# Optimization experiments

Measured on AMD Instinct MI355X. Metric: run time of the kernel, lower is better.

The kernel has to match this reference:

```python
import jax, jax.numpy as jnp
import numpy as np

B, T, D, H, N = 16, 512, 256, 4, 10
DK = D // H
EPS = 1e-12  # espnet LayerNorm eps


def _pe(t, d):
    # espnet PositionalEncoding table
    pos = np.arange(t, dtype=np.float32)[:, None]
    div = np.exp(np.arange(0, d, 2, dtype=np.float32) * (-np.log(10000.0) / d))
    pe = np.zeros((t, d), dtype=np.float32)
    pe[:, 0::2] = np.sin(pos * div)
    pe[:, 1::2] = np.cos(pos * div)
    return jnp.asarray(pe)


def _ln(x, g, b):
    m = jnp.mean(x, -1, keepdims=True)
    v = jnp.var(x, -1, keepdims=True)
    return (x - m) * jax.lax.rsqrt(v + EPS) * g + b


def _forward(x, x_lengths, lids, Wq, bq, Wk, bk, Wv, bv, Wo, bo, W1, b1, W2, b2, g1, be1, g2, be2, gf, bef):
    b, t, d = x.shape
    pe = _pe(t, d)
    pad = jnp.arange(t)[None, :] < x_lengths[:, None]          # [b,t] non-pad mask
    amask = pad[:, None, None, :]                               # [b,1,1,t] key mask
    onehot = (lids[:, None] == jnp.arange(N)[None, :]).astype(x.dtype)  # [b,N]
    h0 = x * np.float32(np.sqrt(d)) + pe[None]                  # scaled input + pos-enc (shared across experts)
    neg = jnp.finfo(x.dtype).min
    out = jnp.zeros_like(x)
    for z in range(N):  # fixed small set of structurally-distinct experts
        # pre-norm self-attention block
        hn = _ln(h0, g1[z], be1[z])
        q = (hn @ Wq[z] + bq[z]).reshape(b, t, H, DK).transpose(0, 2, 1, 3)
        k_ = (hn @ Wk[z] + bk[z]).reshape(b, t, H, DK).transpose(0, 2, 1, 3)
        v_ = (hn @ Wv[z] + bv[z]).reshape(b, t, H, DK).transpose(0, 2, 1, 3)
        scores = jnp.einsum('bhqd,bhkd->bhqk', q, k_) / np.float32(np.sqrt(DK))
        attn = jax.nn.softmax(jnp.where(amask, scores, neg), axis=-1)
        attn = jnp.where(amask, attn, jnp.zeros((), x.dtype))
        ctx = jnp.einsum('bhqk,bhkd->bhqd', attn, v_).transpose(0, 2, 1, 3).reshape(b, t, d)
        h = h0 + ctx @ Wo[z] + bo[z]
        # pre-norm feed-forward block
        hn2 = _ln(h, g2[z], be2[z])
        h = h + jax.nn.relu(hn2 @ W1[z] + b1[z]) @ W2[z] + b2[z]
        # final after_norm, then one-hot masked combine (== emb_lang sum)
        out = out + onehot[:, z, None, None] * _ln(h, gf[z], bef[z])
    return out


def setup_inputs() -> dict:
    key = jax.random.key(0)
    ks = jax.random.split(key, 12)
    s = np.float32(0.02)
    FF = 4 * D
    return {
        'x': jax.random.normal(ks[0], (B, T, D), jnp.float32),
        'x_lengths': jax.random.randint(ks[1], (B,), T // 2, T + 1),
        'lids': jax.random.randint(ks[2], (B,), 0, N),
        'Wq': jax.random.normal(ks[3], (N, D, D), jnp.float32) * s,
        'bq': jnp.zeros((N, D), jnp.float32),
        'Wk': jax.random.normal(ks[4], (N, D, D), jnp.float32) * s,
        'bk': jnp.zeros((N, D), jnp.float32),
        'Wv': jax.random.normal(ks[5], (N, D, D), jnp.float32) * s,
        'bv': jnp.zeros((N, D), jnp.float32),
        'Wo': jax.random.normal(ks[6], (N, D, D), jnp.float32) * s,
        'bo': jnp.zeros((N, D), jnp.float32),
        'W1': jax.random.normal(ks[7], (N, D, FF), jnp.float32) * s,
        'b1': jnp.zeros((N, FF), jnp.float32),
        'W2': jax.random.normal(ks[8], (N, FF, D), jnp.float32) * s,
        'b2': jnp.zeros((N, D), jnp.float32),
        'g1': jnp.ones((N, D), jnp.float32),
        'be1': jnp.zeros((N, D), jnp.float32),
        'g2': jnp.ones((N, D), jnp.float32),
        'be2': jnp.zeros((N, D), jnp.float32),
        'gf': jnp.ones((N, D), jnp.float32),
        'bef': jnp.zeros((N, D), jnp.float32),
    }


def reference(x, x_lengths, lids, Wq, bq, Wk, bk, Wv, bv, Wo, bo, W1, b1, W2, b2, g1, be1, g2, be2, gf, bef):
    return _forward(x, x_lengths, lids, Wq, bq, Wk, bk, Wv, bv, Wo, bo, W1, b1, W2, b2, g1, be1, g2, be2, gf, bef)
```

## Files before the change

kernel.cpp:

```cpp
#include <hip/hip_runtime.h>

typedef unsigned short u16;
typedef __bf16 bf16x8 __attribute__((ext_vector_type(8)));
typedef float  f32x4  __attribute__((ext_vector_type(4)));
typedef unsigned int   u32x4 __attribute__((ext_vector_type(4)));
typedef unsigned short u16x4 __attribute__((ext_vector_type(4)));

#define DEV __device__ __forceinline__

#define NB   16
#define TT   512
#define DD   256
#define HH   4
#define DKH  64
#define NLANG 10
#define FFD  1024

DEV u16 f2bf(float f) {
  unsigned int u = __builtin_bit_cast(unsigned int, f);
  return (u16)((u + 0x7fffu + ((u >> 16) & 1u)) >> 16);
}

DEV f32x4 zero4() { f32x4 z; z[0]=0.f; z[1]=0.f; z[2]=0.f; z[3]=0.f; return z; }

typedef __attribute__((address_space(1))) const unsigned int g_as1;
typedef __attribute__((address_space(3))) unsigned int l_as3;
DEV void load_lds16(const void* g, void* l) {
  __builtin_amdgcn_global_load_lds((g_as1*)g, (l_as3*)l, 16, 0, 0);
}

__global__ __launch_bounds__(256) void pre_kernel(
    const float* __restrict__ Wq, const float* __restrict__ Wk,
    const float* __restrict__ Wv, const float* __restrict__ Wo,
    const float* __restrict__ W1, const float* __restrict__ W2,
    u16* __restrict__ wtq, u16* __restrict__ wtk, u16* __restrict__ wtv,
    u16* __restrict__ wto, u16* __restrict__ wt1, u16* __restrict__ wt2,
    const float* __restrict__ x, float* __restrict__ h0, u16* __restrict__ hn,
    const float* __restrict__ g, const float* __restrict__ be,
    const int* __restrict__ lids) {
  __shared__ u16 tile[32][33];
  const int bx = blockIdx.x;
  if (bx < 7680) {
    const float* src; u16* dst; int R, C, z, r0, c0;
    if (bx < 2560) {
      const int w = bx / 640, rem = bx % 640;
      src = (w == 0) ? Wq : (w == 1) ? Wk : (w == 2) ? Wv : Wo;
      dst = (w == 0) ? wtq : (w == 1) ? wtk : (w == 2) ? wtv : wto;
      R = 256; C = 256; z = rem >> 6;
      const int rc = rem & 63; r0 = (rc >> 3) * 32; c0 = (rc & 7) * 32;
    } else if (bx < 5120) {
      const int rem = bx - 2560; src = W1; dst = wt1; R = 256; C = 1024;
      z = rem >> 8; const int rc = rem & 255; r0 = (rc >> 5) * 32; c0 = (rc & 31) * 32;
    } else {
      const int rem = bx - 5120; src = W2; dst = wt2; R = 1024; C = 256;
      z = rem >> 8; const int rc = rem & 255; r0 = (rc >> 3) * 32; c0 = (rc & 7) * 32;
    }
    const float* s = src + (size_t)z * R * C;
    u16* d = dst + (size_t)z * R * C;
    const int tx = threadIdx.x & 31, ty = threadIdx.x >> 5;
#pragma unroll
    for (int rr = 0; rr < 4; ++rr) {
      const int r = ty + rr * 8;
      tile[r][tx] = f2bf(s[(size_t)(r0 + r) * C + c0 + tx]);
    }
    __syncthreads();
#pragma unroll
    for (int rr = 0; rr < 4; ++rr) {
      const int cc = ty + rr * 8;
      d[(size_t)(c0 + cc) * R + r0 + tx] = tile[tx][cc];
    }
  } else {
    const int wave = threadIdx.x >> 6, lane = threadIdx.x & 63;
    const int row = (bx - 7680) * 4 + wave;
    const int b = row >> 9, t = row & 511;
    const int z = lids[b];
    const int c0 = lane * 4;
    const float4 xv = *(const float4*)(x + (size_t)row * DD + c0);
    const float kPE = -9.21034037197618f / 256.0f;
    float div0 = __expf(kPE * (float)c0);
    float div1 = __expf(kPE * (float)(c0 + 2));
    float a0 = div0 * (float)t, a1 = div1 * (float)t;
    float h[4];
    h[0] = xv.x * 16.0f + sinf(a0);
    h[1] = xv.y * 16.0f + cosf(a0);
    h[2] = xv.z * 16.0f + sinf(a1);
    h[3] = xv.w * 16.0f + cosf(a1);
    float s = h[0] + h[1] + h[2] + h[3];
    float ss = h[0]*h[0] + h[1]*h[1] + h[2]*h[2] + h[3]*h[3];
#pragma unroll
    for (int d = 1; d < 64; d <<= 1) { s += __shfl_xor(s, d); ss += __shfl_xor(ss, d); }
    float mean = s * (1.0f / 256.0f);
    float var  = ss * (1.0f / 256.0f) - mean * mean;
    float rstd = rsqrtf(var + 1e-12f);
    *(float4*)(h0 + (size_t)row * DD + c0) = make_float4(h[0], h[1], h[2], h[3]);
    u16x4 o;
#pragma unroll
    for (int j = 0; j < 4; ++j)
      o[j] = f2bf((h[j] - mean) * rstd * g[z * DD + c0 + j] + be[z * DD + c0 + j]);
    *(u16x4*)(hn + (size_t)row * DD + c0) = o;
  }
}

template<int OUTF32>
__global__ __launch_bounds__(256) void ln_kernel(const float* __restrict__ in,
                                                 void* __restrict__ outp,
                                                 const float* __restrict__ g,
                                                 const float* __restrict__ be,
                                                 const int* __restrict__ lids) {
  const int wave = threadIdx.x >> 6, lane = threadIdx.x & 63;
  const int row = blockIdx.x * 4 + wave;
  const int b = row >> 9;
  const int z = lids[b];
  const int c0 = lane * 4;
  const float4 v = *(const float4*)(in + (size_t)row * DD + c0);
  float h[4] = {v.x, v.y, v.z, v.w};
  float s = h[0] + h[1] + h[2] + h[3];
  float ss = h[0]*h[0] + h[1]*h[1] + h[2]*h[2] + h[3]*h[3];
#pragma unroll
  for (int d = 1; d < 64; d <<= 1) { s += __shfl_xor(s, d); ss += __shfl_xor(ss, d); }
  float mean = s * (1.0f / 256.0f);
  float var  = ss * (1.0f / 256.0f) - mean * mean;
  float rstd = rsqrtf(var + 1e-12f);
  if (OUTF32) {
    float4 o;
    o.x = (h[0] - mean) * rstd * g[z * DD + c0 + 0] + be[z * DD + c0 + 0];
    o.y = (h[1] - mean) * rstd * g[z * DD + c0 + 1] + be[z * DD + c0 + 1];
    o.z = (h[2] - mean) * rstd * g[z * DD + c0 + 2] + be[z * DD + c0 + 2];
    o.w = (h[3] - mean) * rstd * g[z * DD + c0 + 3] + be[z * DD + c0 + 3];
    *(float4*)((float*)outp + (size_t)row * DD + c0) = o;
  } else {
    u16x4 o;
#pragma unroll
    for (int j = 0; j < 4; ++j)
      o[j] = f2bf((h[j] - mean) * rstd * g[z * DD + c0 + j] + be[z * DD + c0 + j]);
    *(u16x4*)((u16*)outp + (size_t)row * DD + c0) = o;
  }
}

DEV void gemm_tile(const u16* __restrict__ A, const u16* __restrict__ W, int K,
                   int m0, int n0, u16* Alds, u16* Blds, f32x4 acc[4][4]) {
  const int tid = threadIdx.x;
  const int lane = tid & 63;
  const int wave = tid >> 6;
  const int wm = wave >> 1, wn = wave & 1;
  const int l15 = lane & 15, lhi = lane >> 4;
  const int srow = tid >> 3;
  const int sc8 = (tid & 7) << 3;
  for (int k0 = 0; k0 < K; k0 += 64) {
#pragma unroll
    for (int it = 0; it < 4; ++it) {
      int r = srow + it * 32;
      *(u32x4*)(Alds + r * 72 + sc8) = *(const u32x4*)(A + (size_t)(m0 + r) * K + k0 + sc8);
      *(u32x4*)(Blds + r * 72 + sc8) = *(const u32x4*)(W + (size_t)(n0 + r) * K + k0 + sc8);
    }
    __syncthreads();
#pragma unroll
    for (int ks = 0; ks < 2; ++ks) {
      const int kk = ks * 32 + lhi * 8;
      bf16x8 af[4], bfr[4];
#pragma unroll
      for (int m = 0; m < 4; ++m)
        af[m] = *(const bf16x8*)(Alds + (wm * 64 + m * 16 + l15) * 72 + kk);
#pragma unroll
      for (int n = 0; n < 4; ++n)
        bfr[n] = *(const bf16x8*)(Blds + (wn * 64 + n * 16 + l15) * 72 + kk);
#pragma unroll
      for (int m = 0; m < 4; ++m)
#pragma unroll
        for (int n = 0; n < 4; ++n)
          acc[m][n] = __builtin_amdgcn_mfma_f32_16x16x32_bf16(af[m], bfr[n], acc[m][n], 0, 0, 0);
    }
    __syncthreads();
  }
}

template<int EPI>
__global__ __launch_bounds__(256) void gemm_kernel(const u16* __restrict__ A,
                                                   const u16* __restrict__ Wt,
                                                   const float* __restrict__ bias,
                                                   const float* __restrict__ res,
                                                   void* __restrict__ outp,
                                                   const int* __restrict__ lids,
                                                   int N, int K) {
  __shared__ u16 Alds[128 * 72];
  __shared__ u16 Blds[128 * 72];
  const int b = blockIdx.z;
  const int z = lids[b];
  const int m0 = blockIdx.y * 128, n0 = blockIdx.x * 128;
  f32x4 acc[4][4];
#pragma unroll
  for (int i = 0; i < 4; ++i)
#pragma unroll
    for (int j = 0; j < 4; ++j) acc[i][j] = zero4();
  gemm_tile(A + (size_t)b * TT * K, Wt + (size_t)z * N * K, K, m0, n0, Alds, Blds, acc);
  const int lane = threadIdx.x & 63, wave = threadIdx.x >> 6;
  const int wm = wave >> 1, wn = wave & 1;
  const int l15 = lane & 15, lhi = lane >> 4;
  float bvv[4];
#pragma unroll
  for (int n = 0; n < 4; ++n) bvv[n] = bias[(size_t)z * N + n0 + wn * 64 + n * 16 + l15];
#pragma unroll
  for (int m = 0; m < 4; ++m) {
    const int grow = m0 + wm * 64 + m * 16 + lhi * 4;
#pragma unroll
    for (int n = 0; n < 4; ++n) {
      const int gcol = n0 + wn * 64 + n * 16 + l15;
#pragma unroll
      for (int r = 0; r < 4; ++r) {
        float v = acc[m][n][r] + bvv[n];
        size_t idx = (size_t)b * TT * N + (size_t)(grow + r) * N + gcol;
        if (EPI == 1) ((u16*)outp)[idx] = f2bf(v > 0.f ? v : 0.f);
        else ((u16*)outp)[idx] = f2bf(v);
      }
    }
  }
}

__global__ __launch_bounds__(256) void gemm64_kernel(const u16* __restrict__ A,
                                                     const u16* __restrict__ Wt,
                                                     const float* __restrict__ bias,
                                                     const float* __restrict__ res,
                                                     float* __restrict__ outp,
                                                     const int* __restrict__ lids,
                                                     int N, int K) {
  __shared__ u16 Alds[128 * 72];
  __shared__ u16 Blds[64 * 72];
  const int b = blockIdx.z;
  const int z = lids[b];
  const int m0 = blockIdx.y * 128, n0 = blockIdx.x * 64;
  const int tid = threadIdx.x, lane = tid & 63, wave = tid >> 6;
  const int l15 = lane & 15, lhi = lane >> 4;
  const int srow = tid >> 3, sc8 = (tid & 7) << 3;
  const u16* Ab = A + (size_t)b * TT * K;
  const u16* Wb = Wt + (size_t)z * N * K;
  f32x4 acc[2][4];
#pragma unroll
  for (int i = 0; i < 2; ++i)
#pragma unroll
    for (int j = 0; j < 4; ++j) acc[i][j] = zero4();
  for (int k0 = 0; k0 < K; k0 += 64) {
#pragma unroll
    for (int it = 0; it < 4; ++it) {
      int r = srow + it * 32;
      *(u32x4*)(Alds + r * 72 + sc8) = *(const u32x4*)(Ab + (size_t)(m0 + r) * K + k0 + sc8);
    }
#pragma unroll
    for (int it = 0; it < 2; ++it) {
      int r = srow + it * 32;
      *(u32x4*)(Blds + r * 72 + sc8) = *(const u32x4*)(Wb + (size_t)(n0 + r) * K + k0 + sc8);
    }
    __syncthreads();
#pragma unroll
    for (int ks = 0; ks < 2; ++ks) {
      const int kk = ks * 32 + lhi * 8;
      bf16x8 af[2], bfr[4];
#pragma unroll
      for (int m = 0; m < 2; ++m)
        af[m] = *(const bf16x8*)(Alds + (wave * 32 + m * 16 + l15) * 72 + kk);
#pragma unroll
      for (int n = 0; n < 4; ++n)
        bfr[n] = *(const bf16x8*)(Blds + (n * 16 + l15) * 72 + kk);
#pragma unroll
      for (int m = 0; m < 2; ++m)
#pragma unroll
        for (int n = 0; n < 4; ++n)
          acc[m][n] = __builtin_amdgcn_mfma_f32_16x16x32_bf16(af[m], bfr[n], acc[m][n], 0, 0, 0);
    }
    __syncthreads();
  }
  float bvv[4];
#pragma unroll
  for (int n = 0; n < 4; ++n) bvv[n] = bias[(size_t)z * N + n0 + n * 16 + l15];
#pragma unroll
  for (int m = 0; m < 2; ++m) {
    const int grow = m0 + wave * 32 + m * 16 + lhi * 4;
#pragma unroll
    for (int n = 0; n < 4; ++n) {
      const int gcol = n0 + n * 16 + l15;
#pragma unroll
      for (int r = 0; r < 4; ++r) {
        size_t idx = (size_t)b * TT * N + (size_t)(grow + r) * N + gcol;
        outp[idx] = res[idx] + acc[m][n][r] + bvv[n];
      }
    }
  }
}

__global__ __launch_bounds__(256) void gemm_qkv(const u16* __restrict__ A,
                                                const u16* __restrict__ wtq,
                                                const u16* __restrict__ wtk,
                                                const u16* __restrict__ wtv,
                                                const float* __restrict__ bq,
                                                const float* __restrict__ bk,
                                                const float* __restrict__ bv,
                                                u16* __restrict__ qo,
                                                u16* __restrict__ ko,
                                                u16* __restrict__ vto,
                                                const int* __restrict__ lids) {
  __shared__ u16 Alds[128 * 72];
  __shared__ u16 Blds[128 * 72];
  const int b = blockIdx.z & 15, which = blockIdx.z >> 4;
  const int z = lids[b];
  const u16* W = (which == 0) ? wtq : (which == 1) ? wtk : wtv;
  const float* bias = (which == 0) ? bq : (which == 1) ? bk : bv;
  const int m0 = blockIdx.y * 128, n0 = blockIdx.x * 128;
  f32x4 acc[4][4];
#pragma unroll
  for (int i = 0; i < 4; ++i)
#pragma unroll
    for (int j = 0; j < 4; ++j) acc[i][j] = zero4();
  gemm_tile(A + (size_t)b * TT * DD, W + (size_t)z * DD * DD, DD, m0, n0, Alds, Blds, acc);
  const int lane = threadIdx.x & 63, wave = threadIdx.x >> 6;
  const int wm = wave >> 1, wn = wave & 1;
  const int l15 = lane & 15, lhi = lane >> 4;
  float bvv[4];
#pragma unroll
  for (int n = 0; n < 4; ++n) bvv[n] = bias[(size_t)z * DD + n0 + wn * 64 + n * 16 + l15];
  if (which < 2) {
    u16* out = (which == 0) ? qo : ko;
#pragma unroll
    for (int m = 0; m < 4; ++m) {
      const int grow = m0 + wm * 64 + m * 16 + lhi * 4;
#pragma unroll
      for (int n = 0; n < 4; ++n) {
        const int gcol = n0 + wn * 64 + n * 16 + l15;
#pragma unroll
        for (int r = 0; r < 4; ++r)
          out[(size_t)b * TT * DD + (size_t)(grow + r) * DD + gcol] = f2bf(acc[m][n][r] + bvv[n]);
      }
    }
  } else {
#pragma unroll
    for (int m = 0; m < 4; ++m) {
      const int grow = m0 + wm * 64 + m * 16 + lhi * 4;
#pragma unroll
      for (int n = 0; n < 4; ++n) {
        const int gcol = n0 + wn * 64 + n * 16 + l15;
        u16x4 pk;
#pragma unroll
        for (int r = 0; r < 4; ++r) pk[r] = f2bf(acc[m][n][r] + bvv[n]);
        *(u16x4*)(vto + (size_t)(b * HH + (gcol >> 6)) * DKH * TT + (size_t)(gcol & 63) * TT + grow) = pk;
      }
    }
  }
}

__global__ __launch_bounds__(512, 4) void attn_kernel(const u16* __restrict__ q,
                                                      const u16* __restrict__ k,
                                                      const u16* __restrict__ vt,
                                                      u16* __restrict__ ctx,
                                                      const int* __restrict__ lens) {
  __shared__ char smem[65536];
  u16* Kbuf = (u16*)smem;
  u16* Pbuf = (u16*)(smem + 32768);
  float* Of = (float*)smem;
  float* Ml = (float*)(smem + 32768);
  float* Ll = (float*)(smem + 32768 + 256);

  const int qt = blockIdx.x, h = blockIdx.y, b = blockIdx.z;
  const int tid = threadIdx.x;
  const int lane = tid & 63, wave = tid >> 6;
  const int grp = wave >> 2, wq = wave & 3;
  const int l15 = lane & 15, lhi = lane >> 4;
  const int len = lens[b];
  const int nt = (len + 127) >> 7;
  const int iters = (nt + 1) >> 1;
  const int qrow0 = qt * 64 + wq * 16;
  const u16* qb = q + (size_t)b * TT * DD + h * DKH;
  const u16* kb = k + (size_t)b * TT * DD + h * DKH;
  const u16* vtb = vt + (size_t)(b * HH + h) * DKH * TT;
  const float SC = 0.125f * 1.4426950408889634f;

  u16* Kg = Kbuf + grp * (128 * 64);
  u16* Pg = Pbuf + grp * (64 * 128);

  bf16x8 qf[2];
#pragma unroll
  for (int ks = 0; ks < 2; ++ks)
    qf[ks] = *(const bf16x8*)(qb + (size_t)(qrow0 + l15) * DD + ks * 32 + lhi * 8);

  auto stage = [&](int t) {
    const int r0w = wq * 32;
#pragma unroll
    for (int j = 0; j < 4; ++j) {
      const int rb = r0w + j * 8;
      const int r = rb + (lane >> 3);
      const int s = (lane & 7) ^ (r & 7);
      load_lds16(kb + (size_t)(t * 128 + r) * DD + s * 8, Kg + rb * 64);
    }
  };

  float m[4] = {-1e30f, -1e30f, -1e30f, -1e30f};
  float l[4] = {0.f, 0.f, 0.f, 0.f};
  f32x4 o[4];
#pragma unroll
  for (int d0 = 0; d0 < 4; ++d0) o[d0] = zero4();

  stage(grp);

  for (int i = 0; i < iters; ++i) {
    __syncthreads();
    const int t = 2 * i + grp;
    const bool active = (t < nt);
    if (active) {
      f32x4 S[8];
#pragma unroll
      for (int nb = 0; nb < 8; ++nb) {
        f32x4 a = zero4();
#pragma unroll
        for (int ks = 0; ks < 2; ++ks) {
          const int row = nb * 16 + l15;
          const int swz = (ks * 64 + lhi * 16) ^ ((row & 7) << 4);
          bf16x8 kf = *(const bf16x8*)(Kg + row * 64 + (swz >> 1));
          a = __builtin_amdgcn_mfma_f32_16x16x32_bf16(qf[ks], kf, a, 0, 0, 0);
        }
        S[nb] = a;
      }
      float tmax[4] = {-1e30f, -1e30f, -1e30f, -1e30f};
#pragma unroll
      for (int nb = 0; nb < 8; ++nb) {
        const int col = t * 128 + nb * 16 + l15;
#pragma unroll
        for (int r = 0; r < 4; ++r) {
          float v = S[nb][r] * SC;
          v = (col < len) ? v : -1e30f;
          S[nb][r] = v;
          tmax[r] = fmaxf(tmax[r], v);
        }
      }
#pragma unroll
      for (int d = 1; d < 16; d <<= 1)
#pragma unroll
        for (int r = 0; r < 4; ++r) tmax[r] = fmaxf(tmax[r], __shfl_xor(tmax[r], d));
      float al[4];
#pragma unroll
      for (int r = 0; r < 4; ++r) {
        float mn = fmaxf(m[r], tmax[r]);
        al[r] = exp2f(m[r] - mn);
        m[r] = mn;
      }
      float rs[4] = {0.f, 0.f, 0.f, 0.f};
#pragma unroll
      for (int nb = 0; nb < 8; ++nb) {
#pragma unroll
        for (int r = 0; r < 4; ++r) {
          float p = exp2f(S[nb][r] - m[r]);
          rs[r] += p;
          const int lrow = wq * 16 + lhi * 4 + r;
          const int swzb = ((nb * 16 + l15) * 2) ^ ((lrow & 7) << 4);
          Pg[(lrow * 256 + swzb) >> 1] = f2bf(p);
        }
      }
#pragma unroll
      for (int d = 1; d < 16; d <<= 1)
#pragma unroll
        for (int r = 0; r < 4; ++r) rs[r] += __shfl_xor(rs[r], d);
#pragma unroll
      for (int r = 0; r < 4; ++r) l[r] = l[r] * al[r] + rs[r];
#pragma unroll
      for (int d0 = 0; d0 < 4; ++d0)
#pragma unroll
        for (int r = 0; r < 4; ++r) o[d0][r] *= al[r];
    }
    __syncthreads();
    if (t + 2 < nt) stage(t + 2);
    if (active) {
      const int arow = wq * 16 + l15;
#pragma unroll
      for (int ks = 0; ks < 4; ++ks) {
        const int swz = (ks * 64 + lhi * 16) ^ ((arow & 7) << 4);
        bf16x8 pf = *(const bf16x8*)(Pg + arow * 128 + (swz >> 1));
#pragma unroll
        for (int d0 = 0; d0 < 4; ++d0) {
          bf16x8 vf = *(const bf16x8*)(vtb + (size_t)(d0 * 16 + l15) * TT + t * 128 + ks * 32 + lhi * 8);
          o[d0] = __builtin_amdgcn_mfma_f32_16x16x32_bf16(pf, vf, o[d0], 0, 0, 0);
        }
      }
    }
  }

  __syncthreads();
  if (grp == 1) {
#pragma unroll
    for (int d0 = 0; d0 < 4; ++d0)
#pragma unroll
      for (int r = 0; r < 4; ++r)
        Of[(wq * 16 + lhi * 4 + r) * 68 + d0 * 16 + l15] = o[d0][r];
    if (l15 == 0) {
#pragma unroll
      for (int r = 0; r < 4; ++r) {
        Ml[wq * 16 + lhi * 4 + r] = m[r];
        Ll[wq * 16 + lhi * 4 + r] = l[r];
      }
    }
  }
  __syncthreads();
  if (grp == 0) {
    u16* cb = ctx + (size_t)b * TT * DD + h * DKH;
#pragma unroll
    for (int r = 0; r < 4; ++r) {
      const int lrow = wq * 16 + lhi * 4 + r;
      const float m1 = Ml[lrow], l1 = Ll[lrow];
      const float mn = fmaxf(m[r], m1);
      const float a0 = exp2f(m[r] - mn), a1 = exp2f(m1 - mn);
      const float linv = 1.0f / (l[r] * a0 + l1 * a1);
#pragma unroll
      for (int d0 = 0; d0 < 4; ++d0) {
        const float of = Of[lrow * 68 + d0 * 16 + l15];
        const float out = (o[d0][r] * a0 + of * a1) * linv;
        cb[(size_t)(qt * 64 + lrow) * DD + d0 * 16 + l15] = f2bf(out);
      }
    }
  }
}

extern "C" void kernel_launch(void* const* d_in, const int* in_sizes, int n_in,
                              void* d_out, int out_size, void* d_ws, size_t ws_size,
                              hipStream_t stream) {
  (void)in_sizes; (void)n_in; (void)out_size; (void)ws_size;
  const float* x    = (const float*)d_in[0];
  const int*   xlen = (const int*)d_in[1];
  const int*   lids = (const int*)d_in[2];
  const float* Wq = (const float*)d_in[3];
  const float* bq = (const float*)d_in[4];
  const float* Wk = (const float*)d_in[5];
  const float* bk = (const float*)d_in[6];
  const float* Wv = (const float*)d_in[7];
  const float* bv = (const float*)d_in[8];
  const float* Wo = (const float*)d_in[9];
  const float* bo = (const float*)d_in[10];
  const float* W1 = (const float*)d_in[11];
  const float* b1 = (const float*)d_in[12];
  const float* W2 = (const float*)d_in[13];
  const float* b2 = (const float*)d_in[14];
  const float* g1 = (const float*)d_in[15];
  const float* be1= (const float*)d_in[16];
  const float* g2 = (const float*)d_in[17];
  const float* be2= (const float*)d_in[18];
  const float* gf = (const float*)d_in[19];
  const float* bef= (const float*)d_in[20];

  char* ws = (char*)d_ws;
  size_t off = 0;
  auto alloc = [&](size_t bytes) -> void* {
    void* p = ws + off;
    off = (off + bytes + 255) & ~(size_t)255;
    return p;
  };
  u16* wtq = (u16*)alloc((size_t)NLANG * DD * DD * 2);
  u16* wtk = (u16*)alloc((size_t)NLANG * DD * DD * 2);
  u16* wtv = (u16*)alloc((size_t)NLANG * DD * DD * 2);
  u16* wto = (u16*)alloc((size_t)NLANG * DD * DD * 2);
  u16* wt1 = (u16*)alloc((size_t)NLANG * DD * FFD * 2);
  u16* wt2 = (u16*)alloc((size_t)NLANG * FFD * DD * 2);
  float* h0 = (float*)alloc((size_t)NB * TT * DD * 4);
  float* hc = (float*)alloc((size_t)NB * TT * DD * 4);
  u16* hn  = (u16*)alloc((size_t)NB * TT * DD * 2);
  u16* qb  = (u16*)alloc((size_t)NB * TT * DD * 2);
  u16* kb  = (u16*)alloc((size_t)NB * TT * DD * 2);
  u16* vtb = (u16*)alloc((size_t)NB * TT * DD * 2);
  u16* ctx = (u16*)alloc((size_t)NB * TT * DD * 2);
  u16* ffn = (u16*)alloc((size_t)NB * TT * FFD * 2);

  pre_kernel<<<dim3(7680 + 2048), 256, 0, stream>>>(
      Wq, Wk, Wv, Wo, W1, W2, wtq, wtk, wtv, wto, wt1, wt2,
      x, h0, hn, g1, be1, lids);

  gemm_qkv<<<dim3(2, 4, 48), 256, 0, stream>>>(hn, wtq, wtk, wtv, bq, bk, bv, qb, kb, vtb, lids);

  attn_kernel<<<dim3(8, HH, NB), 512, 0, stream>>>(qb, kb, vtb, ctx, xlen);

  gemm64_kernel<<<dim3(4, 4, NB), 256, 0, stream>>>(ctx, wto, bo, h0, hc, lids, DD, DD);

  ln_kernel<0><<<dim3(NB * TT / 4), 256, 0, stream>>>(hc, hn, g2, be2, lids);

  gemm_kernel<1><<<dim3(8, 4, NB), 256, 0, stream>>>(hn, wt1, b1, nullptr, ffn, lids, FFD, DD);

  gemm64_kernel<<<dim3(4, 4, NB), 256, 0, stream>>>(ffn, wt2, b2, hc, hc, lids, DD, FFD);

  ln_kernel<1><<<dim3(NB * TT / 4), 256, 0, stream>>>(hc, d_out, gf, bef, lids);
}
```

Before: 105.8 us.

## Use direct global-to-LDS loads with XOR swizzle and skip unused expert weight conversion

GEMM tiles are now loaded with global_load_lds, which writes directly into LDS without going through registers. The padded 72-stride layout is replaced by an unpadded 64-stride layout with an XOR swizzle to keep fragment reads free of bank conflicts. The weight transpose/convert pre-pass also skips experts that no batch row's language ID selects, cutting conversion work for unused weights. The swizzled addressing must match between the load and read paths, and unconverted expert buffers stay stale, which is harmless only because nothing reads them.

```diff
diff --git a/kernel.cpp b/kernel.cpp
--- a/kernel.cpp
+++ b/kernel.cpp
@@ -27,6 +27,10 @@
 typedef __attribute__((address_space(3))) unsigned int l_as3;
 DEV void load_lds16(const void* g, void* l) {
   __builtin_amdgcn_global_load_lds((g_as1*)g, (l_as3*)l, 16, 0, 0);
+}
+
+DEV bf16x8 lds_frag(const u16* lds, int row, int slot) {
+  return *(const bf16x8*)(lds + row * 64 + ((slot ^ (row & 7)) << 3));
 }
 
 __global__ __launch_bounds__(256) void pre_kernel(
@@ -55,6 +59,10 @@
       const int rem = bx - 5120; src = W2; dst = wt2; R = 1024; C = 256;
       z = rem >> 8; const int rc = rem & 255; r0 = (rc >> 3) * 32; c0 = (rc & 7) * 32;
     }
+    bool used = false;
+#pragma unroll
+    for (int i = 0; i < NB; ++i) used |= (lids[i] == z);
+    if (!used) return;
     const float* s = src + (size_t)z * R * C;
     u16* d = dst + (size_t)z * R * C;
     const int tx = threadIdx.x & 31, ty = threadIdx.x >> 5;
@@ -144,26 +152,31 @@
   const int wave = tid >> 6;
   const int wm = wave >> 1, wn = wave & 1;
   const int l15 = lane & 15, lhi = lane >> 4;
-  const int srow = tid >> 3;
-  const int sc8 = (tid & 7) << 3;
+  const int lr = lane >> 3, lsl = lane & 7;
+  const u16* srcA[4]; const u16* srcB[4];
+#pragma unroll
+  for (int j = 0; j < 4; ++j) {
+    const int r = wave * 32 + j * 8 + lr;
+    srcA[j] = A + (size_t)(m0 + r) * K + ((lsl ^ (r & 7)) << 3);
+    srcB[j] = W + (size_t)(n0 + r) * K + ((lsl ^ (r & 7)) << 3);
+  }
   for (int k0 = 0; k0 < K; k0 += 64) {
 #pragma unroll
-    for (int it = 0; it < 4; ++it) {
-      int r = srow + it * 32;
-      *(u32x4*)(Alds + r * 72 + sc8) = *(const u32x4*)(A + (size_t)(m0 + r) * K + k0 + sc8);
-      *(u32x4*)(Blds + r * 72 + sc8) = *(const u32x4*)(W + (size_t)(n0 + r) * K + k0 + sc8);
+    for (int j = 0; j < 4; ++j) {
+      load_lds16(srcA[j] + k0, Alds + (wave * 32 + j * 8) * 64);
+      load_lds16(srcB[j] + k0, Blds + (wave * 32 + j * 8) * 64);
     }
     __syncthreads();
 #pragma unroll
     for (int ks = 0; ks < 2; ++ks) {
-      const int kk = ks * 32 + lhi * 8;
+      const int slot = ks * 4 + lhi;
       bf16x8 af[4], bfr[4];
 #pragma unroll
       for (int m = 0; m < 4; ++m)
-        af[m] = *(const bf16x8*)(Alds + (wm * 64 + m * 16 + l15) * 72 + kk);
+        af[m] = lds_frag(Alds, wm * 64 + m * 16 + l15, slot);
 #pragma unroll
       for (int n = 0; n < 4; ++n)
-        bfr[n] = *(const bf16x8*)(Blds + (wn * 64 + n * 16 + l15) * 72 + kk);
+        bfr[n] = lds_frag(Blds, wn * 64 + n * 16 + l15, slot);
 #pragma unroll
       for (int m = 0; m < 4; ++m)
 #pragma unroll
@@ -182,8 +195,8 @@
                                                    void* __restrict__ outp,
                                                    const int* __restrict__ lids,
                                                    int N, int K) {
-  __shared__ u16 Alds[128 * 72];
-  __shared__ u16 Blds[128 * 72];
+  __shared__ u16 Alds[128 * 64];
+  __shared__ u16 Blds[128 * 64];
   const int b = blockIdx.z;
   const int z = lids[b];
   const int m0 = blockIdx.y * 128, n0 = blockIdx.x * 128;
@@ -223,16 +236,27 @@
                                                      float* __restrict__ outp,
                                                      const int* __restrict__ lids,
                                                      int N, int K) {
-  __shared__ u16 Alds[128 * 72];
-  __shared__ u16 Blds[64 * 72];
+  __shared__ u16 Alds[128 * 64];
+  __shared__ u16 Blds[64 * 64];
   const int b = blockIdx.z;
   const int z = lids[b];
   const int m0 = blockIdx.y * 128, n0 = blockIdx.x * 64;
   const int tid = threadIdx.x, lane = tid & 63, wave = tid >> 6;
   const int l15 = lane & 15, lhi = lane >> 4;
-  const int srow = tid >> 3, sc8 = (tid & 7) << 3;
+  const int lr = lane >> 3, lsl = lane & 7;
   const u16* Ab = A + (size_t)b * TT * K;
   const u16* Wb = Wt + (size_t)z * N * K;
+  const u16* srcA[4]; const u16* srcB[2];
+#pragma unroll
+  for (int j = 0; j < 4; ++j) {
+    const int r = wave * 32 + j * 8 + lr;
+    srcA[j] = Ab + (size_t)(m0 + r) * K + ((lsl ^ (r & 7)) << 3);
+  }
+#pragma unroll
+  for (int j = 0; j < 2; ++j) {
+    const int r = wave * 16 + j * 8 + lr;
+    srcB[j] = Wb + (size_t)(n0 + r) * K + ((lsl ^ (r & 7)) << 3);
+  }
   f32x4 acc[2][4];
 #pragma unroll
   for (int i = 0; i < 2; ++i)
@@ -240,26 +264,22 @@
     for (int j = 0; j < 4; ++j) acc[i][j] = zero4();
   for (int k0 = 0; k0 < K; k0 += 64) {
 #pragma unroll
-    for (int it = 0; it < 4; ++it) {
-      int r = srow + it * 32;
-      *(u32x4*)(Alds + r * 72 + sc8) = *(const u32x4*)(Ab + (size_t)(m0 + r) * K + k0 + sc8);
-    }
-#pragma unroll
-    for (int it = 0; it < 2; ++it) {
-      int r = srow + it * 32;
-      *(u32x4*)(Blds + r * 72 + sc8) = *(const u32x4*)(Wb + (size_t)(n0 + r) * K + k0 + sc8);
-    }
+    for (int j = 0; j < 4; ++j)
+      load_lds16(srcA[j] + k0, Alds + (wave * 32 + j * 8) * 64);
+#pragma unroll
+    for (int j = 0; j < 2; ++j)
+      load_lds16(srcB[j] + k0, Blds + (wave * 16 + j * 8) * 64);
     __syncthreads();
 #pragma unroll
     for (int ks = 0; ks < 2; ++ks) {
-      const int kk = ks * 32 + lhi * 8;
+      const int slot = ks * 4 + lhi;
       bf16x8 af[2], bfr[4];
 #pragma unroll
       for (int m = 0; m < 2; ++m)
-        af[m] = *(const bf16x8*)(Alds + (wave * 32 + m * 16 + l15) * 72 + kk);
+        af[m] = lds_frag(Alds, wave * 32 + m * 16 + l15, slot);
 #pragma unroll
       for (int n = 0; n < 4; ++n)
-        bfr[n] = *(const bf16x8*)(Blds + (n * 16 + l15) * 72 + kk);
+        bfr[n] = lds_frag(Blds, n * 16 + l15, slot);
 #pragma unroll
       for (int m = 0; m < 2; ++m)
 #pragma unroll
@@ -297,8 +317,8 @@
                                                 u16* __restrict__ ko,
                                                 u16* __restrict__ vto,
                                                 const int* __restrict__ lids) {
-  __shared__ u16 Alds[128 * 72];
-  __shared__ u16 Blds[128 * 72];
+  __shared__ u16 Alds[128 * 64];
+  __shared__ u16 Blds[128 * 64];
   const int b = blockIdx.z & 15, which = blockIdx.z >> 4;
   const int z = lids[b];
   const u16* W = (which == 0) ? wtq : (which == 1) ? wtk : wtv;
```

New measurement: 105.2 us. About the same (-0.6%).
